# Kernel tuning notes

Measured on AMD Instinct MI355X. Metric: run time of the kernel, lower is better.

The kernel has to match this reference:

```python
import jax, jax.numpy as jnp
import numpy as np

SCALE = 2
RGB_RANGE = 255.0
RGB_MEAN = jnp.array([0.4488, 0.4371, 0.404], dtype=jnp.float32)


def _conv(x, w, b):
    # x: (N,C,H,W), w: (O,I,3,3)
    y = jax.lax.conv_general_dilated(
        x, w, window_strides=(1, 1), padding='SAME',
        dimension_numbers=('NCHW', 'OIHW', 'NCHW'))
    return y + b[None, :, None, None]


def setup_inputs() -> dict:
    key = jax.random.key(0)
    ks = jax.random.split(key, 16)
    N, H, W, C = 4, 256, 256, 16
    P = SCALE * SCALE * H * W
    inp = {
        'x': jax.random.uniform(ks[0], (N, 3, H, W), dtype=jnp.float32),
        'pos_mat': jax.random.uniform(ks[1], (1, P, 3), dtype=jnp.float32),
        'c0w': jax.random.normal(ks[2], (C, 3, 3, 3), dtype=jnp.float32) * 0.1,
        'c0b': jnp.zeros((C,), dtype=jnp.float32),
        'c1w': jax.random.normal(ks[3], (C, C, 3, 3), dtype=jnp.float32) * 0.05,
        'c1b': jnp.zeros((C,), dtype=jnp.float32),
        'c2w': jax.random.normal(ks[4], (C, C, 3, 3), dtype=jnp.float32) * 0.05,
        'c2b': jnp.zeros((C,), dtype=jnp.float32),
        'c3w': jax.random.normal(ks[5], (C, C, 3, 3), dtype=jnp.float32) * 0.05,
        'c3b': jnp.zeros((C,), dtype=jnp.float32),
        # Pos2Weight MLP: Linear(3,256) -> ReLU -> Linear(256, 3*3*16*3=432)
        'w1': jax.random.normal(ks[6], (3, 256), dtype=jnp.float32) * 0.3,
        'b1': jnp.zeros((256,), dtype=jnp.float32),
        'w2': jax.random.normal(ks[7], (256, 3 * 3 * C * 3), dtype=jnp.float32) * 0.05,
        'b2': jnp.zeros((3 * 3 * C * 3,), dtype=jnp.float32),
    }
    return inp


def reference(x, pos_mat, c0w, c0b, c1w, c1b, c2w, c2b, c3w, c3b, w1, b1, w2, b2):
    N = x.shape[0]
    s = SCALE
    # feature CNN
    f = jax.nn.relu(_conv(x, c0w, c0b))
    f = jax.nn.relu(_conv(f, c1w, c1b))
    f = jax.nn.relu(_conv(f, c2w, c2b))
    f = jax.nn.relu(_conv(f, c3w, c3b))  # (N,16,H,W)
    C, H, W = f.shape[1], f.shape[2], f.shape[3]

    # Pos2Weight MLP on (P,3) positions
    pos = pos_mat.reshape(pos_mat.shape[1], -1)          # (P,3)
    h = jax.nn.relu(pos @ w1 + b1)
    lw = h @ w2 + b2                                     # (P, 9*C*3)
    # torch: view(H, s, W, s, 9*C, 3).permute(1,3,0,2,4,5) -> (s^2, H*W, 9*C, 3)
    lw = lw.reshape(H, s, W, s, 9 * C, 3)
    lw = lw.transpose(1, 3, 0, 2, 4, 5).reshape(s * s, H * W, 9 * C, 3)

    # unfold 3x3 pad 1 (torch ordering: channel-major, then kh, kw).
    # repeat_x just tiles identical copies of f s^2 times, so compute cols once.
    xp = jnp.pad(f, ((0, 0), (0, 0), (1, 1), (1, 1)))
    patches = jnp.stack([xp[:, :, i:i + H, j:j + W]
                         for i in range(3) for j in range(3)], axis=2)  # (N,C,9,H,W)
    cols = patches.reshape(N, C * 9, H * W).transpose(0, 2, 1)          # (N, H*W, 9*C)

    # per-pixel locally-connected matmul: (1,9C) @ (9C,3) at each (q,p)
    out = jnp.einsum('nps,qpsc->nqpc', cols, lw)         # (N, s^2, H*W, 3)
    out = out.transpose(0, 1, 3, 2)                      # (N, s^2, 3, H*W)
    out = out.reshape(N, s, s, 3, H, W).transpose(0, 3, 4, 1, 5, 2)
    out = out.reshape(N, 3, s * H, s * W)

    # add_mean (MeanShift sign=+1, std=1): add rgb_range*mean per channel
    out = out + (RGB_RANGE * RGB_MEAN)[None, :, None, None]
    return out
```

## Files before the change

kernel.cpp:

```cpp
#include <hip/hip_runtime.h>
#include <string.h>

typedef _Float16 half2v __attribute__((ext_vector_type(2)));
typedef _Float16 half4  __attribute__((ext_vector_type(4)));
typedef _Float16 half8  __attribute__((ext_vector_type(8)));
typedef float    float4v __attribute__((ext_vector_type(4)));
typedef unsigned int uint4v __attribute__((ext_vector_type(4)));

#define HH 256
#define WW 256

static __device__ inline half2v pkrtz(float a, float b) {
    return __builtin_bit_cast(half2v, __builtin_amdgcn_cvt_pkrtz(a, b));
}

static __device__ inline float fdot2f(half2v a, half2v b, float c) {
#if __has_builtin(__builtin_amdgcn_fdot2)
    return __builtin_amdgcn_fdot2(__builtin_bit_cast(__fp16 __attribute__((ext_vector_type(2))), a),
                                  __builtin_bit_cast(__fp16 __attribute__((ext_vector_type(2))), b),
                                  c, false);
#else
    return c + (float)a[0] * (float)b[0] + (float)a[1] * (float)b[1];
#endif
}

__global__ __launch_bounds__(256) void xcvt(
    const float* __restrict__ x, _Float16* __restrict__ xh)
{
    int gid = blockIdx.x * 256 + threadIdx.x;
    int px = gid & 65535, n = gid >> 16;
    float r = x[n * 196608 + px];
    float g = x[n * 196608 + 65536 + px];
    float b = x[n * 196608 + 131072 + px];
    half2v p0 = pkrtz(r, g);
    half2v p1 = pkrtz(b, 0.f);
    unsigned u0, u1;
    memcpy(&u0, &p0, 4); memcpy(&u1, &p1, 4);
    uint4v v0 = {u0, u1, 0u, 0u};
    uint4v v1 = {0u, 0u, 0u, 0u};
    uint4v* dst = (uint4v*)&xh[(long)gid * 16];
    dst[0] = v0; dst[1] = v1;
}

__global__ __launch_bounds__(256) void pack_wc(
    const float* __restrict__ w0, const float* __restrict__ w1c,
    const float* __restrict__ w2c, const float* __restrict__ w3c,
    half8* __restrict__ wpk)
{
    int tid = blockIdx.x * 256 + threadIdx.x;
    if (tid >= 1280) return;
    int l = tid & 63, s = (tid >> 6) % 5, cv = tid / 320;
    const float* w = (cv == 0) ? w0 : (cv == 1) ? w1c : (cv == 2) ? w2c : w3c;
    int CIN = (cv == 0) ? 3 : 16;
    int o = l & 15, hi = l >> 4;
    half8 h;
#pragma unroll
    for (int j = 0; j < 8; ++j) {
        int k = 32 * s + hi * 8 + j;
        int tap = k >> 4, ci = k & 15;
        float v = 0.f;
        if (tap < 9 && ci < CIN)
            v = w[((o * CIN + ci) * 3 + tap / 3) * 3 + tap % 3];
        h[j] = (_Float16)v;
    }
    wpk[tid] = h;
}

__global__ __launch_bounds__(256) void conv_mfma(
    const _Float16* __restrict__ in, const half8* __restrict__ wpk,
    const float* __restrict__ bias, _Float16* __restrict__ outp)
{
    __shared__ _Float16 tile[7][66][16];

    const int t = threadIdx.x;
    const int bid = blockIdx.x;
    const int xt = bid & 3, yt = (bid >> 2) & 63, n = bid >> 8;
    const int x0 = xt * 64, y0 = yt * 4;

    for (int e = t; e < 462; e += 256) {
        int xx = e % 66, row = e / 66;
        int gy = y0 + row - 1, gx = x0 + xx - 1;
        uint4v v0 = {0u,0u,0u,0u}, v1 = {0u,0u,0u,0u};
        if (gy >= 0 && gy < HH && gx >= 0 && gx < WW) {
            const uint4v* src = (const uint4v*)&in[(((long)(n*HH+gy))*WW + gx) * 16];
            v0 = src[0]; v1 = src[1];
        }
        uint4v* dst = (uint4v*)&tile[row][xx][0];
        dst[0] = v0; dst[1] = v1;
    }
    __syncthreads();

    const int wid = t >> 6, lane = t & 63;
    const int l15 = lane & 15, hi = lane >> 4;

    half8 af[5];
#pragma unroll
    for (int s = 0; s < 5; ++s) af[s] = wpk[s * 64 + lane];
    const float4v bini = *(const float4v*)&bias[hi * 4];

    const int ty = wid;
    const half8* bp = (const half8*)&tile[0][0][0];
#pragma unroll
    for (int tx = 0; tx < 4; ++tx) {
        float4v acc = bini;
#pragma unroll
        for (int s = 0; s < 5; ++s) {
            int tap = 2 * s + (hi >> 1);
            int dyq = (tap * 11) >> 5;
            int dxr = tap - dyq * 3;
            int cell = (ty + dyq) * 66 + (tx * 16 + l15 + dxr);
            half8 bf = bp[cell * 2 + (hi & 1)];
            acc = __builtin_amdgcn_mfma_f32_16x16x32_f16(af[s], bf, acc, 0, 0, 0);
        }
        int gx = x0 + tx * 16 + l15, gy = y0 + ty;
        half2v p0 = pkrtz(fmaxf(acc[0], 0.f), fmaxf(acc[1], 0.f));
        half2v p1 = pkrtz(fmaxf(acc[2], 0.f), fmaxf(acc[3], 0.f));
        half4 ov = __builtin_shufflevector(p0, p1, 0, 1, 2, 3);
        *(half4*)&outp[(((long)(n*HH+gy))*WW + gx) * 16 + hi * 4] = ov;
    }
}

__global__ __launch_bounds__(256) void pack_w2(
    const float* __restrict__ w2, const float* __restrict__ b2,
    half8* __restrict__ w2p, float* __restrict__ b2p)
{
    int tid = blockIdx.x * 256 + threadIdx.x;
    int l  = tid & 63;
    int s  = (tid >> 6) & 7;
    int tt = tid >> 9;
    int kk = tt / 3, c = tt % 3;
    int ci = l & 15;
    int col = (ci * 9 + kk) * 3 + c;
    int kbase = s * 32 + (l >> 4) * 8;
    half8 h;
#pragma unroll
    for (int j = 0; j < 8; ++j)
        h[j] = (_Float16)w2[(kbase + j) * 432 + col];
    w2p[tid] = h;

    if (tid < 432) {
        int tt2 = tid >> 4, ci2 = tid & 15;
        int kk2 = tt2 / 3, c2 = tt2 % 3;
        b2p[tid] = b2[(ci2 * 9 + kk2) * 3 + c2];
    }
}

__global__ __launch_bounds__(512, 4) void mlp_lc_mfma(
    const float* __restrict__ pos, const float* __restrict__ w1,
    const float* __restrict__ b1,  const half8* __restrict__ w2p,
    const float* __restrict__ b2p, const _Float16* __restrict__ f,
    float* __restrict__ out)
{
    __shared__ __attribute__((aligned(16))) char smem[47872];
    _Float16* h_lds    = (_Float16*)smem;
    _Float16* f_lds    = (_Float16*)(smem + 33792);
    float*    pos_lds  = (float*)(smem + 33792 + 13056);
    float*    part_lds = (float*)smem;

    const int t = threadIdx.x;
    const int bid = blockIdx.x;
    const int lb  = (bid & 7) * 512 + (bid >> 3);
    const int p0  = lb * 64;
    const int t2  = p0 >> 9;
    const int hh  = t2 >> 1;
    const int ww0 = (p0 >> 1) & (WW - 1);

    if (t < 192) pos_lds[(t / 3) * 4 + (t % 3)] = pos[p0 * 3 + t];

    if (t < 408) {
        int x = t % 34, nd = t / 34;
        int dy = nd % 3, n = nd / 3;
        int gy = hh + dy - 1, gx = ww0 + x - 1;
        uint4v v0 = {0u,0u,0u,0u}, v1 = {0u,0u,0u,0u};
        if (gy >= 0 && gy < HH && gx >= 0 && gx < WW) {
            const uint4v* src = (const uint4v*)&f[(((long)(n*HH+gy))*WW + gx) * 16];
            v0 = src[0]; v1 = src[1];
        }
        int cell = (((dy * 34 + x) * 4) + n) ^ (x & 7);
        uint4v* dst = (uint4v*)&f_lds[cell * 16];
        dst[0] = v0; dst[1] = v1;
    }
    __syncthreads();

    {
        const int k  = t & 255;
        const int i0 = (t >> 8) * 32;
        float wa = w1[k], wb = w1[256 + k], wc = w1[512 + k], bb = b1[k];
#pragma unroll 8
        for (int i = i0; i < i0 + 32; ++i) {
            float4v pv = *(const float4v*)&pos_lds[i * 4];
            float a = fmaf(pv[0], wa, fmaf(pv[1], wb, fmaf(pv[2], wc, bb)));
            h_lds[i * 264 + k] = (_Float16)fmaxf(a, 0.f);
        }
    }
    __syncthreads();

    const int wid  = t >> 6;
    const int lane = t & 63;
    const int l15  = lane & 15, hi = lane >> 4;
    const int tb   = (wid <= 3) ? wid * 4 : 12 + (wid - 3) * 3;
    const int cnt  = (wid < 3) ? 4 : 3;

    float4v acc[4][4];
#pragma unroll
    for (int tt = 0; tt < 4; ++tt)
        if (tt < cnt) {
            float4v binit = *(const float4v*)&b2p[(tb + tt) * 16 + hi * 4];
#pragma unroll
            for (int pg = 0; pg < 4; ++pg) acc[tt][pg] = binit;
        }

    for (int ks = 0; ks < 8; ++ks) {
        half8 bfrag[4];
#pragma unroll
        for (int pg = 0; pg < 4; ++pg)
            bfrag[pg] = *(const half8*)&h_lds[(pg * 16 + l15) * 264 + ks * 32 + hi * 8];
#pragma unroll
        for (int tt = 0; tt < 4; ++tt)
            if (tt < cnt) {
                half8 afrag = w2p[((tb + tt) * 8 + ks) * 64 + lane];
#pragma unroll
                for (int pg = 0; pg < 4; ++pg)
                    acc[tt][pg] = __builtin_amdgcn_mfma_f32_16x16x32_f16(
                        afrag, bfrag[pg], acc[tt][pg], 0, 0, 0);
            }
    }
    __syncthreads();

    const int r3 = tb % 3;
    int dy_t[4], dx_t[4];
#pragma unroll
    for (int tt = 0; tt < 4; ++tt) {
        int kk = (tb + tt) / 3;
        dy_t[tt] = kk / 3;
        dx_t[tt] = kk % 3;
    }

#pragma unroll
    for (int pg = 0; pg < 4; ++pg) {
        const int posl = pg * 16 + l15;
        const int xloc = posl >> 1;

        float part[4][3];
#pragma unroll
        for (int n = 0; n < 4; ++n)
#pragma unroll
            for (int c = 0; c < 3; ++c) part[n][c] = 0.f;

#pragma unroll
        for (int tt = 0; tt < 4; ++tt)
            if (tt < cnt) {
                int x    = xloc + dx_t[tt];
                int key  = x & 7;
                int b4   = (dy_t[tt] * 34 + x) * 4;
                int basc = ((b4 ^ (key & 4)) << 4) + hi * 4;
                int kn3  = (key & 3) << 4;
                half2v ap = pkrtz(acc[tt][pg][0], acc[tt][pg][1]);
                half2v bq = pkrtz(acc[tt][pg][2], acc[tt][pg][3]);
                const int u = tt % 3;
#pragma unroll
                for (int n = 0; n < 4; ++n) {
                    half4 fv = *(const half4*)&f_lds[basc + ((n << 4) ^ kn3)];
                    half2v flo = __builtin_shufflevector(fv, fv, 0, 1);
                    half2v fhi = __builtin_shufflevector(fv, fv, 2, 3);
                    part[n][u] = fdot2f(flo, ap, fdot2f(fhi, bq, part[n][u]));
                }
            }

        float real[4][3];
        if (r3 == 0) {
#pragma unroll
            for (int n = 0; n < 4; ++n) {
                real[n][0] = part[n][0]; real[n][1] = part[n][1]; real[n][2] = part[n][2];
            }
        } else if (r3 == 1) {
#pragma unroll
            for (int n = 0; n < 4; ++n) {
                real[n][1] = part[n][0]; real[n][2] = part[n][1]; real[n][0] = part[n][2];
            }
        } else {
#pragma unroll
            for (int n = 0; n < 4; ++n) {
                real[n][2] = part[n][0]; real[n][0] = part[n][1]; real[n][1] = part[n][2];
            }
        }

#pragma unroll
        for (int n = 0; n < 4; ++n)
#pragma unroll
            for (int c = 0; c < 3; ++c) {
                float v = real[n][c];
                v += __shfl_xor(v, 16);
                v += __shfl_xor(v, 32);
                if (hi == 0)
                    part_lds[posl * 106 + (n * 3 + c) * 8 + wid] = v;
            }
    }
    __syncthreads();

    for (int e = t; e < 768; e += 512) {
        int posl = e & 63;
        int j = e >> 6;
        const float* pr = &part_lds[posl * 106 + j * 8];
        float4v v0 = *(const float4v*)pr;
        float4v v1 = *(const float4v*)(pr + 4);
        float v = v0[0] + v0[1] + v0[2] + v0[3] + v1[0] + v1[1] + v1[2] + v1[3];
        int n = j / 3, c = j - 3 * n;
        float mean = (c == 0) ? 114.4440f : (c == 1) ? 111.4605f : 103.0200f;
        out[((n * 3 + c) * 512 + t2) * 512 + (ww0 * 2 + posl)] = v + mean;
    }
}

extern "C" void kernel_launch(void* const* d_in, const int* in_sizes, int n_in,
                              void* d_out, int out_size, void* d_ws, size_t ws_size,
                              hipStream_t stream) {
    const float* x    = (const float*)d_in[0];
    const float* pos  = (const float*)d_in[1];
    const float* c0w  = (const float*)d_in[2];
    const float* c1w  = (const float*)d_in[4];
    const float* c2w  = (const float*)d_in[6];
    const float* c3w  = (const float*)d_in[8];
    const float* c0b  = (const float*)d_in[3];
    const float* c1b  = (const float*)d_in[5];
    const float* c2b  = (const float*)d_in[7];
    const float* c3b  = (const float*)d_in[9];
    const float* w1   = (const float*)d_in[10];
    const float* b1   = (const float*)d_in[11];
    const float* w2   = (const float*)d_in[12];
    const float* b2   = (const float*)d_in[13];
    float* out = (float*)d_out;

    char* ws = (char*)d_ws;
    _Float16* xh = (_Float16*)ws;
    _Float16* fA = (_Float16*)(ws + (8u << 20));
    _Float16* fB = (_Float16*)(ws + (16u << 20));
    half8* w2p   = (half8*)(ws + (24u << 20));
    float* b2p   = (float*)(ws + (24u << 20) + 221184);
    half8* wpk   = (half8*)(ws + (24u << 20) + 221184 + 1728);

    xcvt<<<1024, 256, 0, stream>>>(x, xh);
    pack_wc<<<5, 256, 0, stream>>>(c0w, c1w, c2w, c3w, wpk);
    pack_w2<<<54, 256, 0, stream>>>(w2, b2, w2p, b2p);

    conv_mfma<<<1024, 256, 0, stream>>>(xh, wpk,         c0b, fA);
    conv_mfma<<<1024, 256, 0, stream>>>(fA, wpk + 320,   c1b, fB);
    conv_mfma<<<1024, 256, 0, stream>>>(fB, wpk + 640,   c2b, fA);
    conv_mfma<<<1024, 256, 0, stream>>>(fA, wpk + 960,   c3b, fB);

    mlp_lc_mfma<<<4096, 512, 0, stream>>>(pos, w1, b1, w2p, b2p, fB, out);
}
```

Before: 170.9 us.

## Merge weight-pack kernels, pad LDS stride, reduce partials in packed fp16

Merges the two weight-packing kernels into one launch to save a kernel launch. Changes the h_lds row stride from 264 to 268 halves, aiming to reduce LDS bank conflicts on the MFMA B-fragment loads. Packs partial sums of two batch images into one half2 value, so the cross-lane shuffles and the LDS partial buffer carry half as many words and fewer threads do the final sum. In exchange, the final accumulation runs in fp16 rather than fp32, which lowers output precision and may push error past tolerance.

```diff
diff --git a/kernel.cpp b/kernel.cpp
--- a/kernel.cpp
+++ b/kernel.cpp
@@ -9,6 +9,7 @@
 
 #define HH 256
 #define WW 256
+#define HSTR 268
 
 static __device__ inline half2v pkrtz(float a, float b) {
     return __builtin_bit_cast(half2v, __builtin_amdgcn_cvt_pkrtz(a, b));
@@ -42,28 +43,51 @@
     dst[0] = v0; dst[1] = v1;
 }
 
-__global__ __launch_bounds__(256) void pack_wc(
+__global__ __launch_bounds__(256) void pack_all(
+    const float* __restrict__ w2, const float* __restrict__ b2,
+    half8* __restrict__ w2p, float* __restrict__ b2p,
     const float* __restrict__ w0, const float* __restrict__ w1c,
     const float* __restrict__ w2c, const float* __restrict__ w3c,
     half8* __restrict__ wpk)
 {
     int tid = blockIdx.x * 256 + threadIdx.x;
-    if (tid >= 1280) return;
-    int l = tid & 63, s = (tid >> 6) % 5, cv = tid / 320;
-    const float* w = (cv == 0) ? w0 : (cv == 1) ? w1c : (cv == 2) ? w2c : w3c;
-    int CIN = (cv == 0) ? 3 : 16;
-    int o = l & 15, hi = l >> 4;
-    half8 h;
-#pragma unroll
-    for (int j = 0; j < 8; ++j) {
-        int k = 32 * s + hi * 8 + j;
-        int tap = k >> 4, ci = k & 15;
-        float v = 0.f;
-        if (tap < 9 && ci < CIN)
-            v = w[((o * CIN + ci) * 3 + tap / 3) * 3 + tap % 3];
-        h[j] = (_Float16)v;
-    }
-    wpk[tid] = h;
+    if (tid < 13824) {
+        int l  = tid & 63;
+        int s  = (tid >> 6) & 7;
+        int tt = tid >> 9;
+        int kk = tt / 3, c = tt % 3;
+        int ci = l & 15;
+        int col = (ci * 9 + kk) * 3 + c;
+        int kbase = s * 32 + (l >> 4) * 8;
+        half8 h;
+#pragma unroll
+        for (int j = 0; j < 8; ++j)
+            h[j] = (_Float16)w2[(kbase + j) * 432 + col];
+        w2p[tid] = h;
+
+        if (tid < 432) {
+            int tt2 = tid >> 4, ci2 = tid & 15;
+            int kk2 = tt2 / 3, c2 = tt2 % 3;
+            b2p[tid] = b2[(ci2 * 9 + kk2) * 3 + c2];
+        }
+    } else if (tid < 15104) {
+        int t2 = tid - 13824;
+        int l = t2 & 63, s = (t2 >> 6) % 5, cv = t2 / 320;
+        const float* w = (cv == 0) ? w0 : (cv == 1) ? w1c : (cv == 2) ? w2c : w3c;
+        int CIN = (cv == 0) ? 3 : 16;
+        int o = l & 15, hi = l >> 4;
+        half8 h;
+#pragma unroll
+        for (int j = 0; j < 8; ++j) {
+            int k = 32 * s + hi * 8 + j;
+            int tap = k >> 4, ci = k & 15;
+            float v = 0.f;
+            if (tap < 9 && ci < CIN)
+                v = w[((o * CIN + ci) * 3 + tap / 3) * 3 + tap % 3];
+            h[j] = (_Float16)v;
+        }
+        wpk[t2] = h;
+    }
 }
 
 __global__ __launch_bounds__(256) void conv_mfma(
@@ -120,42 +144,17 @@
     }
 }
 
-__global__ __launch_bounds__(256) void pack_w2(
-    const float* __restrict__ w2, const float* __restrict__ b2,
-    half8* __restrict__ w2p, float* __restrict__ b2p)
-{
-    int tid = blockIdx.x * 256 + threadIdx.x;
-    int l  = tid & 63;
-    int s  = (tid >> 6) & 7;
-    int tt = tid >> 9;
-    int kk = tt / 3, c = tt % 3;
-    int ci = l & 15;
-    int col = (ci * 9 + kk) * 3 + c;
-    int kbase = s * 32 + (l >> 4) * 8;
-    half8 h;
-#pragma unroll
-    for (int j = 0; j < 8; ++j)
-        h[j] = (_Float16)w2[(kbase + j) * 432 + col];
-    w2p[tid] = h;
-
-    if (tid < 432) {
-        int tt2 = tid >> 4, ci2 = tid & 15;
-        int kk2 = tt2 / 3, c2 = tt2 % 3;
-        b2p[tid] = b2[(ci2 * 9 + kk2) * 3 + c2];
-    }
-}
-
 __global__ __launch_bounds__(512, 4) void mlp_lc_mfma(
     const float* __restrict__ pos, const float* __restrict__ w1,
     const float* __restrict__ b1,  const half8* __restrict__ w2p,
     const float* __restrict__ b2p, const _Float16* __restrict__ f,
     float* __restrict__ out)
 {
-    __shared__ __attribute__((aligned(16))) char smem[47872];
+    __shared__ __attribute__((aligned(16))) char smem[48384];
     _Float16* h_lds    = (_Float16*)smem;
-    _Float16* f_lds    = (_Float16*)(smem + 33792);
-    float*    pos_lds  = (float*)(smem + 33792 + 13056);
-    float*    part_lds = (float*)smem;
+    _Float16* f_lds    = (_Float16*)(smem + 34304);
+    float*    pos_lds  = (float*)(smem + 34304 + 13056);
+    unsigned* part_u32 = (unsigned*)smem;
 
     const int t = threadIdx.x;
     const int bid = blockIdx.x;
@@ -164,6 +163,10 @@
     const int t2  = p0 >> 9;
     const int hh  = t2 >> 1;
     const int ww0 = (p0 >> 1) & (WW - 1);
+
+    const int wid  = t >> 6;
+    const int lane = t & 63;
+    const int l15  = lane & 15, hi = lane >> 4;
 
     if (t < 192) pos_lds[(t / 3) * 4 + (t % 3)] = pos[p0 * 3 + t];
 
@@ -190,14 +193,11 @@
         for (int i = i0; i < i0 + 32; ++i) {
             float4v pv = *(const float4v*)&pos_lds[i * 4];
             float a = fmaf(pv[0], wa, fmaf(pv[1], wb, fmaf(pv[2], wc, bb)));
-            h_lds[i * 264 + k] = (_Float16)fmaxf(a, 0.f);
-        }
-    }
-    __syncthreads();
-
-    const int wid  = t >> 6;
-    const int lane = t & 63;
-    const int l15  = lane & 15, hi = lane >> 4;
+            h_lds[i * HSTR + k] = (_Float16)fmaxf(a, 0.f);
+        }
+    }
+    __syncthreads();
+
     const int tb   = (wid <= 3) ? wid * 4 : 12 + (wid - 3) * 3;
     const int cnt  = (wid < 3) ? 4 : 3;
 
@@ -214,7 +214,7 @@
         half8 bfrag[4];
 #pragma unroll
         for (int pg = 0; pg < 4; ++pg)
-            bfrag[pg] = *(const half8*)&h_lds[(pg * 16 + l15) * 264 + ks * 32 + hi * 8];
+            bfrag[pg] = *(const half8*)&h_lds[(pg * 16 + l15) * HSTR + ks * 32 + hi * 8];
 #pragma unroll
         for (int tt = 0; tt < 4; ++tt)
             if (tt < cnt) {
@@ -286,28 +286,34 @@
         }
 
 #pragma unroll
-        for (int n = 0; n < 4; ++n)
+        for (int nh = 0; nh < 2; ++nh)
 #pragma unroll
             for (int c = 0; c < 3; ++c) {
-                float v = real[n][c];
-                v += __shfl_xor(v, 16);
-                v += __shfl_xor(v, 32);
+                half2v v = pkrtz(real[2 * nh][c], real[2 * nh + 1][c]);
+                int u1 = __shfl_xor(__builtin_bit_cast(int, v), 16);
+                v = v + __builtin_bit_cast(half2v, u1);
+                int u2 = __shfl_xor(__builtin_bit_cast(int, v), 32);
+                v = v + __builtin_bit_cast(half2v, u2);
                 if (hi == 0)
-                    part_lds[posl * 106 + (n * 3 + c) * 8 + wid] = v;
-            }
-    }
-    __syncthreads();
-
-    for (int e = t; e < 768; e += 512) {
-        int posl = e & 63;
-        int j = e >> 6;
-        const float* pr = &part_lds[posl * 106 + j * 8];
-        float4v v0 = *(const float4v*)pr;
-        float4v v1 = *(const float4v*)(pr + 4);
-        float v = v0[0] + v0[1] + v0[2] + v0[3] + v1[0] + v1[1] + v1[2] + v1[3];
-        int n = j / 3, c = j - 3 * n;
+                    part_u32[posl * 49 + (nh * 3 + c) * 8 + wid] =
+                        __builtin_bit_cast(unsigned, v);
+            }
+    }
+    __syncthreads();
+
+    if (t < 384) {
+        int posl = t & 63;
+        int pr   = t >> 6;
+        const unsigned* pu = &part_u32[posl * 49 + pr * 8];
+        half2v s = __builtin_bit_cast(half2v, pu[0]);
+#pragma unroll
+        for (int w = 1; w < 8; ++w)
+            s = s + __builtin_bit_cast(half2v, pu[w]);
+        int nh = pr / 3, c = pr - 3 * nh;
         float mean = (c == 0) ? 114.4440f : (c == 1) ? 111.4605f : 103.0200f;
-        out[((n * 3 + c) * 512 + t2) * 512 + (ww0 * 2 + posl)] = v + mean;
+        int ox = ww0 * 2 + posl;
+        out[(((2 * nh) * 3 + c) * 512 + t2) * 512 + ox]     = (float)s[0] + mean;
+        out[(((2 * nh + 1) * 3 + c) * 512 + t2) * 512 + ox] = (float)s[1] + mean;
     }
 }
 
@@ -339,8 +345,7 @@
     half8* wpk   = (half8*)(ws + (24u << 20) + 221184 + 1728);
 
     xcvt<<<1024, 256, 0, stream>>>(x, xh);
-    pack_wc<<<5, 256, 0, stream>>>(c0w, c1w, c2w, c3w, wpk);
-    pack_w2<<<54, 256, 0, stream>>>(w2, b2, w2p, b2p);
+    pack_all<<<59, 256, 0, stream>>>(w2, b2, w2p, b2p, c0w, c1w, c2w, c3w, wpk);
 
     conv_mfma<<<1024, 256, 0, stream>>>(xh, wpk,         c0b, fA);
     conv_mfma<<<1024, 256, 0, stream>>>(fA, wpk + 320,   c1b, fB);
```

After: 213.0 us. 1.25x slower.
